# Performance work log

Hardware: AMD Instinct MI355X
Metric: run time of the kernel (lower is better)

Reference implementation:

```python
import jax, jax.numpy as jnp
import numpy as np

G = 128       # grid_scale (large=True)
SCALE = 7.0   # distance scale

def forward_net(x_flat, grid):
    # x_flat: [N, 3] coords in [-1, 1]; grid: [G, G, G]
    # torch .to(torch.long) truncates toward zero, same as astype(int32)
    idx = (G * ((x_flat + 1.0) * 0.5)).astype(jnp.int32)
    oob = jnp.any((idx >= G) | (idx < 0), axis=-1)          # [N]
    idxc = jnp.clip(idx, 0, G - 1)                           # safe gather indices
    d = grid[idxc[:, 0], idxc[:, 1], idxc[:, 2]]             # [N] gather
    return jnp.where(oob, jnp.zeros_like(d), d)              # masked scatter-back

def setup_inputs() -> dict:
    key = jax.random.key(0)
    k1, k2 = jax.random.split(key)
    bs, ns = 8192, 512
    # uniform in [-1.1, 1.1] so some points fall out of bounds (mask path exercised)
    x = jax.random.uniform(k1, (bs, ns, 3), dtype=jnp.float32, minval=-1.1, maxval=1.1)
    grid = jax.random.normal(k2, (G, G, G), dtype=jnp.float32)
    return {"x": x, "grid": grid}

def reference(x, grid):
    bs, ns, _ = x.shape
    # segment lengths between consecutive samples along each ray, scaled
    seg = jnp.sqrt(jnp.sum((x[:, :-1, :3] - x[:, 1:, :3]) ** 2, axis=2, keepdims=True)) * SCALE
    distances = jnp.concatenate([jnp.ones((bs, 1, 1), dtype=x.dtype), seg], axis=1)  # [bs, ns, 1]
    dens = forward_net(x.reshape(bs * ns, 3), grid).reshape(bs, ns, 1)
    # Beer-Lambert style attenuation
    return jnp.exp(-jnp.sum(dens * distances, axis=1))  # [bs, 1]
```

## Files before the change

kernel.cpp:

```cpp
#include <hip/hip_runtime.h>
#include <math.h>

constexpr int   G     = 128;
constexpr int   NS    = 512;
constexpr float SCALE = 7.0f;

constexpr float OUT_CLAMP = 3.0e38f;

__global__ __launch_bounds__(256) void em_grid_kernel(
    const float* __restrict__ x,
    const float* __restrict__ grid,
    float* __restrict__ out,
    int bs)
{
    const int gtid = blockIdx.x * blockDim.x + threadIdx.x;
    const int row  = gtid >> 6;
    const int lane = threadIdx.x & 63;
    if (row >= bs) return;

    const float* xr = x + (size_t)row * (NS * 3);

    float4 q[6];
    const float4* src = reinterpret_cast<const float4*>(xr + lane * 24);
#pragma unroll
    for (int i = 0; i < 6; ++i) q[i] = src[i];
    const float* v = reinterpret_cast<const float*>(q);

    float px = __shfl_up(v[21], 1);
    float py = __shfl_up(v[22], 1);
    float pz = __shfl_up(v[23], 1);

    double acc = 0.0;
#pragma unroll
    for (int k = 0; k < 8; ++k) {
        const float cx = v[k * 3 + 0];
        const float cy = v[k * 3 + 1];
        const float cz = v[k * 3 + 2];
        const int s = (lane << 3) + k;

        float dist;
        if (s == 0) {
            dist = 1.0f;
        } else {
            const float dx = cx - px, dy = cy - py, dz = cz - pz;
            dist = sqrtf(dx * dx + dy * dy + dz * dz) * SCALE;
        }

        const float fx = (cx + 1.0f) * 0.5f * (float)G;
        const float fy = (cy + 1.0f) * 0.5f * (float)G;
        const float fz = (cz + 1.0f) * 0.5f * (float)G;
        const int ix = (int)fx;
        const int iy = (int)fy;
        const int iz = (int)fz;

        const bool oob = (ix < 0) | (ix >= G) |
                         (iy < 0) | (iy >= G) |
                         (iz < 0) | (iz >= G);

        float d = 0.0f;
        if (!oob) {
            d = grid[(ix * G + iy) * G + iz];
        }

        acc += (double)(d * dist);

        px = cx; py = cy; pz = cz;
    }

#pragma unroll
    for (int off = 1; off < 64; off <<= 1)
        acc += __shfl_xor(acc, off);

    if (lane == 0) {
        float r = expf(-(float)acc);
        if (!(r < OUT_CLAMP)) r = OUT_CLAMP;
        out[row] = r;
    }
}

extern "C" void kernel_launch(void* const* d_in, const int* in_sizes, int n_in,
                              void* d_out, int out_size, void* d_ws, size_t ws_size,
                              hipStream_t stream)
{
    const float* x    = (const float*)d_in[0];
    const float* grid = (const float*)d_in[1];
    float* out        = (float*)d_out;

    const int bs = in_sizes[0] / (NS * 3);

    const int threads = 256;
    const int blocks  = (bs * 64 + threads - 1) / threads;
    em_grid_kernel<<<blocks, threads, 0, stream>>>(x, grid, out, bs);
}
```

Before: 45.86 us.

## Gather from an fp16 copy of the grid and hoist gathers ahead of accumulation

Adds a pre-pass that converts the 8 MB float grid to fp16 in workspace, then gathers from the half-size copy so more of it stays in cache. The eight gathers per lane are hoisted into a separate loop so they can all be in flight at once. Input loads and the output store are made nontemporal so the streamed x does not evict the grid. The cost is an extra kernel launch and a full grid conversion on every call, plus rounding density values to fp16, which changes numerical precision.

```diff
diff --git a/kernel.cpp b/kernel.cpp
--- a/kernel.cpp
+++ b/kernel.cpp
@@ -1,15 +1,33 @@
 #include <hip/hip_runtime.h>
+#include <hip/hip_fp16.h>
 #include <math.h>
 
 constexpr int   G     = 128;
 constexpr int   NS    = 512;
 constexpr float SCALE = 7.0f;
+constexpr int   GRID_ELEMS = G * G * G;
 
 constexpr float OUT_CLAMP = 3.0e38f;
 
+typedef float v4f __attribute__((ext_vector_type(4)));
+
+__global__ __launch_bounds__(256) void grid_to_f16(
+    const v4f* __restrict__ g, ushort4* __restrict__ gh)
+{
+    const int i = blockIdx.x * blockDim.x + threadIdx.x;
+    const v4f f = __builtin_nontemporal_load(g + i);
+    ushort4 o;
+    o.x = __half_as_ushort(__float2half_rn(f.x));
+    o.y = __half_as_ushort(__float2half_rn(f.y));
+    o.z = __half_as_ushort(__float2half_rn(f.z));
+    o.w = __half_as_ushort(__float2half_rn(f.w));
+    gh[i] = o;
+}
+
+template <typename GT>
 __global__ __launch_bounds__(256) void em_grid_kernel(
     const float* __restrict__ x,
-    const float* __restrict__ grid,
+    const GT* __restrict__ grid,
     float* __restrict__ out,
     int bs)
 {
@@ -20,15 +38,31 @@
 
     const float* xr = x + (size_t)row * (NS * 3);
 
-    float4 q[6];
-    const float4* src = reinterpret_cast<const float4*>(xr + lane * 24);
+    v4f q[6];
+    const v4f* src = reinterpret_cast<const v4f*>(xr + lane * 24);
 #pragma unroll
-    for (int i = 0; i < 6; ++i) q[i] = src[i];
+    for (int i = 0; i < 6; ++i) q[i] = __builtin_nontemporal_load(src + i);
     const float* v = reinterpret_cast<const float*>(q);
 
     float px = __shfl_up(v[21], 1);
     float py = __shfl_up(v[22], 1);
     float pz = __shfl_up(v[23], 1);
+
+    float d[8];
+#pragma unroll
+    for (int k = 0; k < 8; ++k) {
+        const float cx = v[k * 3 + 0];
+        const float cy = v[k * 3 + 1];
+        const float cz = v[k * 3 + 2];
+        const int ix = (int)((cx + 1.0f) * 0.5f * (float)G);
+        const int iy = (int)((cy + 1.0f) * 0.5f * (float)G);
+        const int iz = (int)((cz + 1.0f) * 0.5f * (float)G);
+        const bool oob = (ix < 0) | (ix >= G) |
+                         (iy < 0) | (iy >= G) |
+                         (iz < 0) | (iz >= G);
+        d[k] = 0.0f;
+        if (!oob) d[k] = (float)grid[(ix * G + iy) * G + iz];
+    }
 
     double acc = 0.0;
 #pragma unroll
@@ -45,25 +79,7 @@
             const float dx = cx - px, dy = cy - py, dz = cz - pz;
             dist = sqrtf(dx * dx + dy * dy + dz * dz) * SCALE;
         }
-
-        const float fx = (cx + 1.0f) * 0.5f * (float)G;
-        const float fy = (cy + 1.0f) * 0.5f * (float)G;
-        const float fz = (cz + 1.0f) * 0.5f * (float)G;
-        const int ix = (int)fx;
-        const int iy = (int)fy;
-        const int iz = (int)fz;
-
-        const bool oob = (ix < 0) | (ix >= G) |
-                         (iy < 0) | (iy >= G) |
-                         (iz < 0) | (iz >= G);
-
-        float d = 0.0f;
-        if (!oob) {
-            d = grid[(ix * G + iy) * G + iz];
-        }
-
-        acc += (double)(d * dist);
-
+        acc += (double)(d[k] * dist);
         px = cx; py = cy; pz = cz;
     }
 
@@ -74,7 +90,7 @@
     if (lane == 0) {
         float r = expf(-(float)acc);
         if (!(r < OUT_CLAMP)) r = OUT_CLAMP;
-        out[row] = r;
+        __builtin_nontemporal_store(r, &out[row]);
     }
 }
 
@@ -90,5 +106,13 @@
 
     const int threads = 256;
     const int blocks  = (bs * 64 + threads - 1) / threads;
-    em_grid_kernel<<<blocks, threads, 0, stream>>>(x, grid, out, bs);
+
+    if (ws_size >= (size_t)GRID_ELEMS * sizeof(__half)) {
+        __half* gh = (__half*)d_ws;
+        grid_to_f16<<<GRID_ELEMS / 4 / 256, 256, 0, stream>>>(
+            (const v4f*)grid, (ushort4*)gh);
+        em_grid_kernel<__half><<<blocks, threads, 0, stream>>>(x, gh, out, bs);
+    } else {
+        em_grid_kernel<float><<<blocks, threads, 0, stream>>>(x, grid, out, bs);
+    }
 }
```

Measured after the change: 51.03 us. 1.11x slower.
